# Performance work log

Hardware: AMD Instinct MI355X
Metric: run time of the kernel (lower is better)

Reference implementation:

```python
import jax, jax.numpy as jnp
import numpy as np

# ---- fixed sizes ----
N_IN = 100_000          # total inner nodes
NODES_PER_INNER = 50    # nodes per inner graph
N_OUT = N_IN // NODES_PER_INNER          # 2000 outer nodes (= num inner graphs)
NODES_PER_OUTER = 125   # outer nodes per outer graph
B = N_OUT // NODES_PER_OUTER             # 16 graphs in the batch
DEG = 8
E_IN = N_IN * DEG        # 800_000 inner edges
E_OUT = N_OUT * DEG      # 16_000 outer edges
IN_FEATS = 64
OUT_FEATS = 64
H = 128                  # h_feats = [128]*6
NUM_CLASSES = 10


def _rand_edges(key, n_graphs, nodes_per_graph, edges_per_graph):
    """Random edges that stay inside each graph of a batched graph."""
    k1, k2 = jax.random.split(key)
    src_l = jax.random.randint(k1, (n_graphs, edges_per_graph), 0, nodes_per_graph)
    dst_l = jax.random.randint(k2, (n_graphs, edges_per_graph), 0, nodes_per_graph)
    off = (jnp.arange(n_graphs) * nodes_per_graph)[:, None]
    return ((src_l + off).reshape(-1).astype(jnp.int32),
            (dst_l + off).reshape(-1).astype(jnp.int32))


def setup_inputs() -> dict:
    key = jax.random.key(0)
    ks = jax.random.split(key, 24)
    inner_src, inner_dst = _rand_edges(ks[0], N_OUT, NODES_PER_INNER, E_IN // N_OUT)
    outer_src, outer_dst = _rand_edges(ks[1], B, NODES_PER_OUTER, E_OUT // B)

    def w(k, fan_in, fan_out):
        return jax.random.normal(k, (fan_in, fan_out), jnp.float32) * (1.0 / np.sqrt(fan_in))

    inp = {
        "in_layer_feat": jax.random.normal(ks[2], (N_IN, IN_FEATS), jnp.float32),
        "out_layer_feat": jax.random.normal(ks[3], (N_OUT, OUT_FEATS), jnp.float32),
        "inner_ew": jax.random.uniform(ks[4], (E_IN,), jnp.float32) + 0.5,
        "outer_ew": jax.random.uniform(ks[5], (E_OUT,), jnp.float32) + 0.5,
        "W1": w(ks[6], IN_FEATS, H),        "b1": jnp.zeros((H,), jnp.float32),
        "W2": w(ks[7], H, H),               "b2": jnp.zeros((H,), jnp.float32),
        "W3": w(ks[8], OUT_FEATS + H, H),   "b3": jnp.zeros((H,), jnp.float32),
        "W4": w(ks[9], H, H),               "b4": jnp.zeros((H,), jnp.float32),
        "W5": w(ks[10], H, H),              "b5": jnp.zeros((H,), jnp.float32),
        "W6": w(ks[11], H, H),              "b6": jnp.zeros((H,), jnp.float32),
        "Wc": w(ks[12], H, NUM_CLASSES),    "bc": jnp.zeros((NUM_CLASSES,), jnp.float32),
        "inner_src": inner_src, "inner_dst": inner_dst,
        "outer_src": outer_src, "outer_dst": outer_dst,
        "inner_node_graph": (jnp.arange(N_IN) // NODES_PER_INNER).astype(jnp.int32),
        "outer_node_graph": (jnp.arange(N_OUT) // NODES_PER_OUTER).astype(jnp.int32),
    }
    return inp


def graph_conv(src, dst, ew, x, W, b, n_nodes):
    """DGL GraphConv, norm='both', weighted aggregation, zero-in-degree allowed."""
    ones = jnp.ones(src.shape[0], x.dtype)
    deg_out = jnp.clip(jax.ops.segment_sum(ones, src, num_segments=n_nodes), 1.0)
    deg_in = jnp.clip(jax.ops.segment_sum(ones, dst, num_segments=n_nodes), 1.0)
    xs = x * jax.lax.rsqrt(deg_out)[:, None]                      # src normalization
    msg = xs[src] * ew[:, None]                                   # u_mul_e
    agg = jax.ops.segment_sum(msg, dst, num_segments=n_nodes)     # copy_e -> sum
    agg = agg * jax.lax.rsqrt(deg_in)[:, None]                    # dst normalization
    return agg @ W + b


def mean_nodes(h, node_graph, n_graphs, nodes_per_graph):
    return jax.ops.segment_sum(h, node_graph, num_segments=n_graphs) / nodes_per_graph


def reference(in_layer_feat, out_layer_feat, inner_ew, outer_ew,
              W1, b1, W2, b2, W3, b3, W4, b4, W5, b5, W6, b6, Wc, bc,
              inner_src, inner_dst, outer_src, outer_dst,
              inner_node_graph, outer_node_graph):
    # inner-graph message passing
    h = jax.nn.relu(graph_conv(inner_src, inner_dst, inner_ew, in_layer_feat, W1, b1, N_IN))
    h = jax.nn.relu(graph_conv(inner_src, inner_dst, inner_ew, h, W2, b2, N_IN))
    reduced = mean_nodes(h, inner_node_graph, N_OUT, float(NODES_PER_INNER))  # [N_OUT, H]
    merged = jnp.concatenate([out_layer_feat, reduced], axis=-1)              # [N_OUT, OUT_FEATS+H]
    # outer-graph message passing
    h = jax.nn.relu(graph_conv(outer_src, outer_dst, outer_ew, merged, W3, b3, N_OUT))
    h = jax.nn.relu(graph_conv(outer_src, outer_dst, outer_ew, h, W4, b4, N_OUT))
    h = jax.nn.relu(graph_conv(outer_src, outer_dst, outer_ew, h, W5, b5, N_OUT))
    h = jax.nn.relu(graph_conv(outer_src, outer_dst, outer_ew, h, W6, b6, N_OUT))
    hg = mean_nodes(h, outer_node_graph, B, float(NODES_PER_OUTER))           # [B, H]
    return hg @ Wc + bc                                                       # [B, NUM_CLASSES]
```

## Files before the change

kernel.cpp:

```cpp
#include <hip/hip_runtime.h>

#define NPI 50
#define EPI 400
#define NPO 125
#define EPO 1000
#define N_IN 100000
#define N_OUT 2000
#define NB 16
#define NC 10

typedef _Float16 half_t;
typedef _Float16 f16x8 __attribute__((ext_vector_type(8)));
typedef _Float16 f16x4 __attribute__((ext_vector_type(4)));
typedef float f32x4 __attribute__((ext_vector_type(4)));

#define MFMA(a, b, c) __builtin_amdgcn_mfma_f32_16x16x32_f16(a, b, c, 0, 0, 0)

__device__ __forceinline__ void lds_barrier() {
    asm volatile("s_waitcnt lgkmcnt(0)" ::: "memory");
    __builtin_amdgcn_s_barrier();
}

__device__ __forceinline__ f16x8 lds_ld8(const half_t* base, int row, int k, int strideB) {
    return *(const f16x8*)((const char*)base + row * strideB + ((k * 2) ^ ((row & 7) << 4)));
}
__device__ __forceinline__ void lds_st1(half_t* base, int row, int col, int strideB, float v) {
    *(half_t*)((char*)base + row * strideB + ((col * 2) ^ ((row & 7) << 4))) = (half_t)v;
}
__device__ __forceinline__ void lds_st1h(half_t* base, int row, int col, int strideB, half_t v) {
    *(half_t*)((char*)base + row * strideB + ((col * 2) ^ ((row & 7) << 4))) = v;
}
__device__ __forceinline__ void lds_st4h(half_t* base, int row, int col0, int strideB, f16x4 v) {
    *(f16x4*)((char*)base + row * strideB + ((col0 * 2) ^ ((row & 7) << 4))) = v;
}
__device__ __forceinline__ f16x8 scr_ld8(const half_t* base, int row, int k) {
    return *(const f16x8*)((const char*)base + row * 64 + ((k * 2) ^ ((row & 3) << 4)));
}
__device__ __forceinline__ void scr_st1(half_t* base, int row, int col, float v) {
    *(half_t*)((char*)base + row * 64 + ((col * 2) ^ ((row & 3) << 4))) = (half_t)v;
}

__global__ __launch_bounds__(256) void k_pre(
    const float* __restrict__ W1, const float* __restrict__ W2,
    const float* __restrict__ W3, const float* __restrict__ W4,
    const float* __restrict__ W5, const float* __restrict__ W6,
    half_t* __restrict__ WT1, half_t* __restrict__ WT2,
    half_t* __restrict__ WT3, half_t* __restrict__ WT4,
    half_t* __restrict__ WT5, half_t* __restrict__ WT6,
    const float* __restrict__ ew, const int* __restrict__ esrc,
    const int* __restrict__ edst, half_t* __restrict__ Aout)
{
    __shared__ float Af[NPO * NPO];
    __shared__ int cO[NPO], cI[NPO];
    __shared__ float rso[NPO], rsi[NPO];
    const int t = threadIdx.x;

    if (blockIdx.x < 384) {
        int i = blockIdx.x * 256 + t;
        const float* src; half_t* dst; int K;
        if      (i < 8192)  { src = W1; dst = WT1; K = 64; }
        else if (i < 24576) { src = W2; dst = WT2; K = 128; i -= 8192; }
        else if (i < 49152) { src = W3; dst = WT3; K = 192; i -= 24576; }
        else if (i < 65536) { src = W4; dst = WT4; K = 128; i -= 49152; }
        else if (i < 81920) { src = W5; dst = WT5; K = 128; i -= 65536; }
        else                { src = W6; dst = WT6; K = 128; i -= 81920; }
        int c = i & 127, k = i >> 7;
        dst[c * K + k] = (half_t)src[k * 128 + c];
        return;
    }

    const int g = blockIdx.x - 384;
    const int nb = g * NPO, eb = g * EPO;
    for (int i = t; i < NPO * NPO; i += 256) Af[i] = 0.f;
    if (t < NPO) { cO[t] = 0; cI[t] = 0; }
    __syncthreads();
    for (int e = t; e < EPO; e += 256) {
        int s = esrc[eb + e] - nb, d = edst[eb + e] - nb;
        atomicAdd(&Af[d * NPO + s], ew[eb + e]);
        atomicAdd(&cO[s], 1); atomicAdd(&cI[d], 1);
    }
    __syncthreads();
    if (t < NPO) {
        rso[t] = rsqrtf((float)max(cO[t], 1));
        rsi[t] = rsqrtf((float)max(cI[t], 1));
    }
    __syncthreads();
    for (int i = t; i < 128 * 16; i += 256) {
        int d = i >> 4, s0 = (i & 15) * 8;
        f16x8 v;
        #pragma unroll
        for (int j = 0; j < 8; j++) {
            int s = s0 + j;
            float x = (d < NPO && s < NPO) ? Af[d * NPO + s] * rsi[d] * rso[s] : 0.f;
            v[j] = (half_t)x;
        }
        *(f16x8*)&Aout[(size_t)g * 16384 + d * 128 + s0] = v;
    }
}

__global__ __launch_bounds__(256, 5) void k_inner(
    const float* __restrict__ X, const float* __restrict__ outfeat,
    const float* __restrict__ ew, const int* __restrict__ esrc,
    const int* __restrict__ edst,
    const half_t* __restrict__ WT1, const float* __restrict__ b1,
    const half_t* __restrict__ WT2, const float* __restrict__ b2,
    half_t* __restrict__ merged)
{
    __shared__ alignas(16) char smem[21504];
    half_t* R2  = (half_t*)smem;
    float*  Af  = (float*)smem;
    half_t* scr = (half_t*)(smem + 16384);
    float*  pool= (float*)(smem + 20480);
    int*    cO  = (int*)(smem + 20992);
    int*    cI  = (int*)(smem + 21248);

    const int g = blockIdx.x, t = threadIdx.x;
    const int w = t >> 6, l = t & 63, lr = l & 15, lk = l >> 4;
    const int nb = g * NPI, eb = g * EPI;
    half_t* scrw = scr + w * 512;

    float ofv = (t < 64) ? outfeat[(size_t)g * 64 + t] : 0.f;
    int s0e, d0e; float w0e;
    { int e = eb + t; s0e = esrc[e] - nb; d0e = edst[e] - nb; w0e = ew[e]; }
    int s1e = 0, d1e = 0; float w1e = 0.f;
    const bool e1v = (t + 256 < EPI);
    if (e1v) { int e = eb + t + 256; s1e = esrc[e] - nb; d1e = edst[e] - nb; w1e = ew[e]; }
    f16x8 bx[8];
    #pragma unroll
    for (int fi = 0; fi < 4; fi++) {
        #pragma unroll
        for (int ks = 0; ks < 2; ks++) {
            f16x8 v;
            #pragma unroll
            for (int jj = 0; jj < 8; jj++) {
                int n = ks * 32 + lk * 8 + jj;
                int ridx = nb + n; if (ridx > N_IN - 1) ridx = N_IN - 1;
                v[jj] = (half_t)X[(size_t)ridx * 64 + fi * 16 + lr];
            }
            bx[fi * 2 + ks] = v;
        }
    }

    if (t < 64) { cO[t] = 0; cI[t] = 0; }
    if (t >= 64 && t < 192) pool[t - 64] = 0.f;
    {
        const f32x4 z4 = {0.f, 0.f, 0.f, 0.f};
        #pragma unroll
        for (int i = 0; i < 4; i++) *(f32x4*)&Af[(i * 256 + t) * 4] = z4;
    }
    lds_barrier();

    atomicAdd(&Af[d0e * 64 + (s0e ^ ((d0e & 7) << 2))], w0e);
    atomicAdd(&cO[s0e], 1); atomicAdd(&cI[d0e], 1);
    if (e1v) {
        atomicAdd(&Af[d1e * 64 + (s1e ^ ((d1e & 7) << 2))], w1e);
        atomicAdd(&cO[s1e], 1); atomicAdd(&cI[d1e], 1);
    }
    lds_barrier();

    f16x8 afr[2];
    {
        const int r = w * 16 + lr;
        const int sw = (r & 7) << 2;
        const float rsi_l = rsqrtf((float)max(cI[r], 1));
        #pragma unroll
        for (int ks = 0; ks < 2; ks++) {
            const int c0 = ks * 32 + lk * 8;
            f32x4 v0 = *(const f32x4*)&Af[r * 64 + (c0 ^ sw)];
            f32x4 v1 = *(const f32x4*)&Af[r * 64 + ((c0 + 4) ^ sw)];
            f16x8 fr;
            #pragma unroll
            for (int j = 0; j < 4; j++)
                fr[j] = (half_t)(v0[j] * rsi_l * rsqrtf((float)max(cO[c0 + j], 1)));
            #pragma unroll
            for (int j = 0; j < 4; j++)
                fr[4 + j] = (half_t)(v1[j] * rsi_l * rsqrtf((float)max(cO[c0 + 4 + j], 1)));
            afr[ks] = fr;
        }
    }
    lds_barrier();

    f32x4 hacc[8] = {};
    #pragma unroll
    for (int kf = 0; kf < 2; kf++) {
        f16x8 wb[8];
        #pragma unroll
        for (int nt = 0; nt < 8; nt++)
            wb[nt] = *(const f16x8*)&WT1[(nt * 16 + lr) * 64 + kf * 32 + lk * 8];
        #pragma unroll
        for (int j = 0; j < 2; j++) {
            const int ft = kf * 2 + j;
            f32x4 tacc = {};
            #pragma unroll
            for (int ks = 0; ks < 2; ks++)
                tacc = MFMA(afr[ks], bx[ft * 2 + ks], tacc);
            #pragma unroll
            for (int q = 0; q < 4; q++) scr_st1(scrw, lk * 4 + q, j * 16 + lr, tacc[q]);
        }
        f16x8 a1 = scr_ld8(scrw, lr, lk * 8);
        #pragma unroll
        for (int nt = 0; nt < 8; nt++) hacc[nt] = MFMA(a1, wb[nt], hacc[nt]);
    }
    #pragma unroll
    for (int nt = 0; nt < 8; nt++) {
        int c = nt * 16 + lr;
        float bb = b1[c];
        f16x4 hv;
        #pragma unroll
        for (int q = 0; q < 4; q++) hv[q] = (half_t)fmaxf(hacc[nt][q] + bb, 0.f);
        lds_st4h(R2, c, w * 16 + lk * 4, 128, hv);
    }
    lds_barrier();

    f32x4 h2[8] = {};
    #pragma unroll
    for (int kf = 0; kf < 4; kf++) {
        f16x8 wb[8];
        #pragma unroll
        for (int nt = 0; nt < 8; nt++)
            wb[nt] = *(const f16x8*)&WT2[(nt * 16 + lr) * 128 + kf * 32 + lk * 8];
        #pragma unroll
        for (int j = 0; j < 2; j++) {
            const int ft = kf * 2 + j;
            f32x4 tacc = {};
            #pragma unroll
            for (int ks = 0; ks < 2; ks++) {
                f16x8 b = lds_ld8(R2, ft * 16 + lr, ks * 32 + lk * 8, 128);
                tacc = MFMA(afr[ks], b, tacc);
            }
            #pragma unroll
            for (int q = 0; q < 4; q++) scr_st1(scrw, lk * 4 + q, j * 16 + lr, tacc[q]);
        }
        f16x8 a1 = scr_ld8(scrw, lr, lk * 8);
        #pragma unroll
        for (int nt = 0; nt < 8; nt++) h2[nt] = MFMA(a1, wb[nt], h2[nt]);
    }
    #pragma unroll
    for (int nt = 0; nt < 8; nt++) {
        int c = nt * 16 + lr;
        float bb = b2[c];
        float ps = 0.f;
        #pragma unroll
        for (int q = 0; q < 4; q++) {
            int m = w * 16 + lk * 4 + q;
            float v = fmaxf(h2[nt][q] + bb, 0.f);
            ps += (m < NPI) ? v : 0.f;
        }
        ps += __shfl_xor(ps, 16);
        ps += __shfl_xor(ps, 32);
        if (lk == 0) atomicAdd(&pool[c], ps);
    }
    lds_barrier();
    if (t < 64) merged[(size_t)g * 192 + t] = (half_t)ofv;
    else if (t < 192) merged[(size_t)g * 192 + t] = (half_t)(pool[t - 64] * (1.f / NPI));
}

template <int FIN, bool STAGE, bool LAST>
__device__ __forceinline__ void outer_layer(
    const f16x8* afr, const half_t* __restrict__ mg,
    const half_t* __restrict__ WT, const float* __restrict__ bias,
    half_t* bufP, half_t* bufQ, float* pool,
    int wr, int wc, int lr, int lk, int t)
{
    f32x4 hacc[4] = {};
    constexpr int NCH = FIN / 64;
    f16x8 hv[NCH];
    if constexpr (STAGE) {
        const int s = t >> 3, fo = (t & 7) * 8;
        #pragma unroll
        for (int ch = 0; ch < NCH; ch++) {
            f16x8 z = {};
            hv[ch] = (s < NPO) ? *(const f16x8*)&mg[(size_t)s * 192 + ch * 64 + fo] : z;
        }
    }
    #pragma unroll
    for (int ch = 0; ch < NCH; ch++) {
        f16x8 wtb[8];
        #pragma unroll
        for (int ks2 = 0; ks2 < 2; ks2++)
            #pragma unroll
            for (int nt = 0; nt < 4; nt++)
                wtb[ks2 * 4 + nt] = *(const f16x8*)&WT[
                    (size_t)(wc * 64 + nt * 16 + lr) * FIN + ch * 64 + ks2 * 32 + lk * 8];
        if constexpr (STAGE) {
            const int s = t >> 3, fo = (t & 7) * 8;
            #pragma unroll
            for (int j = 0; j < 8; j++) lds_st1h(bufP, fo + j, s, 256, hv[ch][j]);
            lds_barrier();
        }
        const int rb = STAGE ? 0 : ch * 64;
        f32x4 tacc[2] = {};
        #pragma unroll
        for (int ks = 0; ks < 4; ks++) {
            #pragma unroll
            for (int nt = 0; nt < 2; nt++) {
                f16x8 b = lds_ld8(bufP, rb + wc * 32 + nt * 16 + lr, ks * 32 + lk * 8, 256);
                tacc[nt] = MFMA(afr[ks], b, tacc[nt]);
            }
        }
        #pragma unroll
        for (int nt = 0; nt < 2; nt++)
            #pragma unroll
            for (int q = 0; q < 4; q++)
                lds_st1(bufQ, wr * 16 + lk * 4 + q, wc * 32 + nt * 16 + lr, 128,
                        tacc[nt][q]);
        lds_barrier();
        #pragma unroll
        for (int ks2 = 0; ks2 < 2; ks2++) {
            f16x8 a1 = lds_ld8(bufQ, wr * 16 + lr, ks2 * 32 + lk * 8, 128);
            #pragma unroll
            for (int nt = 0; nt < 4; nt++)
                hacc[nt] = MFMA(a1, wtb[ks2 * 4 + nt], hacc[nt]);
        }
        lds_barrier();
    }
    if constexpr (!LAST) {
        #pragma unroll
        for (int nt = 0; nt < 4; nt++) {
            int c = wc * 64 + nt * 16 + lr;
            float bb = bias[c];
            #pragma unroll
            for (int q = 0; q < 4; q++)
                lds_st1(bufP, c, wr * 16 + lk * 4 + q, 256, fmaxf(hacc[nt][q] + bb, 0.f));
        }
        lds_barrier();
    } else {
        #pragma unroll
        for (int nt = 0; nt < 4; nt++) {
            int c = wc * 64 + nt * 16 + lr;
            float bb = bias[c];
            float ps = 0.f;
            #pragma unroll
            for (int q = 0; q < 4; q++) {
                int d = wr * 16 + lk * 4 + q;
                float v = fmaxf(hacc[nt][q] + bb, 0.f);
                ps += (d < NPO) ? v : 0.f;
            }
            ps += __shfl_xor(ps, 16);
            ps += __shfl_xor(ps, 32);
            if (lk == 0) atomicAdd(&pool[c], ps);
        }
        lds_barrier();
    }
}

__global__ __launch_bounds__(1024) void k_outer(
    const half_t* __restrict__ Aout, const half_t* __restrict__ merged,
    const half_t* __restrict__ WT3, const float* __restrict__ b3,
    const half_t* __restrict__ WT4, const float* __restrict__ b4,
    const half_t* __restrict__ WT5, const float* __restrict__ b5,
    const half_t* __restrict__ WT6, const float* __restrict__ b6,
    const float* __restrict__ Wc, const float* __restrict__ bc,
    float* __restrict__ out)
{
    __shared__ alignas(16) char smem[49704];
    half_t* bufP = (half_t*)smem;
    half_t* bufQ = (half_t*)(smem + 32768);
    float*  pool = (float*)(smem + 49152);
    float*  cls  = (float*)(smem + 49664);

    const int g = blockIdx.x, t = threadIdx.x;
    const int w = t >> 6, l = t & 63, lr = l & 15, lk = l >> 4;
    const int wr = w & 7, wc = w >> 3;
    const half_t* mg = merged + (size_t)g * NPO * 192;

    f16x8 afr[4];
    #pragma unroll
    for (int ks = 0; ks < 4; ks++)
        afr[ks] = *(const f16x8*)&Aout[(size_t)g * 16384
                                       + (wr * 16 + lr) * 128 + ks * 32 + lk * 8];
    if (t < 128) pool[t] = 0.f;
    if (t >= 128 && t < 128 + NC) cls[t - 128] = 0.f;
    lds_barrier();

    outer_layer<192, true,  false>(afr, mg, WT3, b3, bufP, bufQ, pool, wr, wc, lr, lk, t);
    outer_layer<128, false, false>(afr, nullptr, WT4, b4, bufP, bufQ, pool, wr, wc, lr, lk, t);
    outer_layer<128, false, false>(afr, nullptr, WT5, b5, bufP, bufQ, pool, wr, wc, lr, lk, t);
    outer_layer<128, false, true >(afr, nullptr, WT6, b6, bufP, bufQ, pool, wr, wc, lr, lk, t);

    if (t < 128) {
        float val = pool[t] * (1.f / NPO);
        float p[NC];
        #pragma unroll
        for (int c = 0; c < NC; c++) p[c] = val * Wc[t * NC + c];
        #pragma unroll
        for (int off = 32; off >= 1; off >>= 1)
            #pragma unroll
            for (int c = 0; c < NC; c++) p[c] += __shfl_xor(p[c], off);
        if ((t & 63) == 0)
            #pragma unroll
            for (int c = 0; c < NC; c++) atomicAdd(&cls[c], p[c]);
    }
    lds_barrier();
    if (t < NC) out[g * NC + t] = cls[t] + bc[t];
}

extern "C" void kernel_launch(void* const* d_in, const int* in_sizes, int n_in,
                              void* d_out, int out_size, void* d_ws, size_t ws_size,
                              hipStream_t stream)
{
    const float* X       = (const float*)d_in[0];
    const float* outfeat = (const float*)d_in[1];
    const float* iew     = (const float*)d_in[2];
    const float* oew     = (const float*)d_in[3];
    const float* W1 = (const float*)d_in[4];  const float* b1 = (const float*)d_in[5];
    const float* W2 = (const float*)d_in[6];  const float* b2 = (const float*)d_in[7];
    const float* W3 = (const float*)d_in[8];  const float* b3 = (const float*)d_in[9];
    const float* W4 = (const float*)d_in[10]; const float* b4 = (const float*)d_in[11];
    const float* W5 = (const float*)d_in[12]; const float* b5 = (const float*)d_in[13];
    const float* W6 = (const float*)d_in[14]; const float* b6 = (const float*)d_in[15];
    const float* Wc = (const float*)d_in[16]; const float* bc = (const float*)d_in[17];
    const int* isrc = (const int*)d_in[18];   const int* idst = (const int*)d_in[19];
    const int* osrc = (const int*)d_in[20];   const int* odst = (const int*)d_in[21];

    char* base = (char*)d_ws;
    half_t* WT1 = (half_t*)(base + 0);
    half_t* WT2 = (half_t*)(base + 16384);
    half_t* WT3 = (half_t*)(base + 49152);
    half_t* WT4 = (half_t*)(base + 98304);
    half_t* WT5 = (half_t*)(base + 131072);
    half_t* WT6 = (half_t*)(base + 163840);
    half_t* AoutG  = (half_t*)(base + 196608);
    half_t* merged = (half_t*)(base + 720896);

    k_pre<<<400, 256, 0, stream>>>(W1, W2, W3, W4, W5, W6,
                                   WT1, WT2, WT3, WT4, WT5, WT6,
                                   oew, osrc, odst, AoutG);
    k_inner<<<N_OUT, 256, 0, stream>>>(X, outfeat, iew, isrc, idst,
                                       WT1, b1, WT2, b2, merged);
    k_outer<<<NB, 1024, 0, stream>>>(AoutG, merged, WT3, b3, WT4, b4,
                                     WT5, b5, WT6, b6, Wc, bc, (float*)d_out);
}
```

Before: 115.9 us.

## Restructure outer-graph layers to per-wave row ownership with private LDS scratch

The outer kernel moves from 1024 threads, split into 8 row waves by 2 column waves, to 512 threads where each wave owns 16 destination rows and all 128 output columns. Each wave writes its aggregated A·H tile to a private padded LDS scratch, so the barriers between the aggregation and weight-multiply stages inside each feature chunk go away. Only one barrier per layer remains around the shared activation buffer. In exchange LDS use roughly doubles, each wave streams the full weight matrix from global memory inside the MFMA loop, and per-block thread parallelism is halved.

```diff
diff --git a/kernel.cpp b/kernel.cpp
--- a/kernel.cpp
+++ b/kernel.cpp
@@ -38,6 +38,12 @@
 }
 __device__ __forceinline__ void scr_st1(half_t* base, int row, int col, float v) {
     *(half_t*)((char*)base + row * 64 + ((col * 2) ^ ((row & 3) << 4))) = (half_t)v;
+}
+__device__ __forceinline__ f16x8 scrS_ld8(const half_t* base, int row, int k, int strideB) {
+    return *(const f16x8*)((const char*)base + row * strideB + ((k * 2) ^ ((row & 3) << 4)));
+}
+__device__ __forceinline__ void scrS_st1(half_t* base, int row, int col, int strideB, float v) {
+    *(half_t*)((char*)base + row * strideB + ((col * 2) ^ ((row & 3) << 4))) = (half_t)v;
 }
 
 __global__ __launch_bounds__(256) void k_pre(
@@ -256,83 +262,67 @@
 }
 
 template <int FIN, bool STAGE, bool LAST>
-__device__ __forceinline__ void outer_layer(
+__device__ __forceinline__ void olayer(
     const f16x8* afr, const half_t* __restrict__ mg,
     const half_t* __restrict__ WT, const float* __restrict__ bias,
-    half_t* bufP, half_t* bufQ, float* pool,
-    int wr, int wc, int lr, int lk, int t)
+    half_t* bufP, half_t* scrw, float* pool,
+    int w, int lr, int lk, int t)
 {
-    f32x4 hacc[4] = {};
-    constexpr int NCH = FIN / 64;
-    f16x8 hv[NCH];
+    constexpr int SSTR = FIN * 2 + 16;
     if constexpr (STAGE) {
-        const int s = t >> 3, fo = (t & 7) * 8;
-        #pragma unroll
-        for (int ch = 0; ch < NCH; ch++) {
-            f16x8 z = {};
-            hv[ch] = (s < NPO) ? *(const f16x8*)&mg[(size_t)s * 192 + ch * 64 + fo] : z;
-        }
-    }
-    #pragma unroll
-    for (int ch = 0; ch < NCH; ch++) {
-        f16x8 wtb[8];
-        #pragma unroll
-        for (int ks2 = 0; ks2 < 2; ks2++)
-            #pragma unroll
-            for (int nt = 0; nt < 4; nt++)
-                wtb[ks2 * 4 + nt] = *(const f16x8*)&WT[
-                    (size_t)(wc * 64 + nt * 16 + lr) * FIN + ch * 64 + ks2 * 32 + lk * 8];
-        if constexpr (STAGE) {
-            const int s = t >> 3, fo = (t & 7) * 8;
-            #pragma unroll
-            for (int j = 0; j < 8; j++) lds_st1h(bufP, fo + j, s, 256, hv[ch][j]);
-            lds_barrier();
-        }
-        const int rb = STAGE ? 0 : ch * 64;
-        f32x4 tacc[2] = {};
+        const int s = t & 127, ch = t >> 7;
+        #pragma unroll
+        for (int j = 0; j < 6; j++) {
+            int f0 = ch * 48 + j * 8;
+            f16x8 hv = {};
+            if (s < NPO) hv = *(const f16x8*)&mg[(size_t)s * 192 + f0];
+            #pragma unroll
+            for (int i = 0; i < 8; i++) lds_st1h(bufP, f0 + i, s, 256, hv[i]);
+        }
+        lds_barrier();
+    }
+    #pragma unroll
+    for (int ft = 0; ft < FIN / 16; ft++) {
+        f32x4 tacc = {};
         #pragma unroll
         for (int ks = 0; ks < 4; ks++) {
-            #pragma unroll
-            for (int nt = 0; nt < 2; nt++) {
-                f16x8 b = lds_ld8(bufP, rb + wc * 32 + nt * 16 + lr, ks * 32 + lk * 8, 256);
-                tacc[nt] = MFMA(afr[ks], b, tacc[nt]);
-            }
-        }
-        #pragma unroll
-        for (int nt = 0; nt < 2; nt++)
+            f16x8 b = lds_ld8(bufP, ft * 16 + lr, ks * 32 + lk * 8, 256);
+            tacc = MFMA(afr[ks], b, tacc);
+        }
+        #pragma unroll
+        for (int q = 0; q < 4; q++)
+            scrS_st1(scrw, lk * 4 + q, ft * 16 + lr, SSTR, tacc[q]);
+    }
+    f32x4 hacc[8] = {};
+    #pragma unroll
+    for (int kf = 0; kf < FIN / 32; kf++) {
+        f16x8 a1 = scrS_ld8(scrw, lr, kf * 32 + lk * 8, SSTR);
+        #pragma unroll
+        for (int nt = 0; nt < 8; nt++) {
+            f16x8 wb = *(const f16x8*)&WT[(size_t)(nt * 16 + lr) * FIN + kf * 32 + lk * 8];
+            hacc[nt] = MFMA(a1, wb, hacc[nt]);
+        }
+    }
+    lds_barrier();
+    if constexpr (!LAST) {
+        #pragma unroll
+        for (int nt = 0; nt < 8; nt++) {
+            int c = nt * 16 + lr;
+            float bb = bias[c];
             #pragma unroll
             for (int q = 0; q < 4; q++)
-                lds_st1(bufQ, wr * 16 + lk * 4 + q, wc * 32 + nt * 16 + lr, 128,
-                        tacc[nt][q]);
-        lds_barrier();
-        #pragma unroll
-        for (int ks2 = 0; ks2 < 2; ks2++) {
-            f16x8 a1 = lds_ld8(bufQ, wr * 16 + lr, ks2 * 32 + lk * 8, 128);
-            #pragma unroll
-            for (int nt = 0; nt < 4; nt++)
-                hacc[nt] = MFMA(a1, wtb[ks2 * 4 + nt], hacc[nt]);
-        }
-        lds_barrier();
-    }
-    if constexpr (!LAST) {
-        #pragma unroll
-        for (int nt = 0; nt < 4; nt++) {
-            int c = wc * 64 + nt * 16 + lr;
-            float bb = bias[c];
-            #pragma unroll
-            for (int q = 0; q < 4; q++)
-                lds_st1(bufP, c, wr * 16 + lk * 4 + q, 256, fmaxf(hacc[nt][q] + bb, 0.f));
+                lds_st1(bufP, c, w * 16 + lk * 4 + q, 256, fmaxf(hacc[nt][q] + bb, 0.f));
         }
         lds_barrier();
     } else {
         #pragma unroll
-        for (int nt = 0; nt < 4; nt++) {
-            int c = wc * 64 + nt * 16 + lr;
+        for (int nt = 0; nt < 8; nt++) {
+            int c = nt * 16 + lr;
             float bb = bias[c];
             float ps = 0.f;
             #pragma unroll
             for (int q = 0; q < 4; q++) {
-                int d = wr * 16 + lk * 4 + q;
+                int d = w * 16 + lk * 4 + q;
                 float v = fmaxf(hacc[nt][q] + bb, 0.f);
                 ps += (d < NPO) ? v : 0.f;
             }
@@ -344,7 +334,7 @@
     }
 }
 
-__global__ __launch_bounds__(1024) void k_outer(
+__global__ __launch_bounds__(512) void k_outer(
     const half_t* __restrict__ Aout, const half_t* __restrict__ merged,
     const half_t* __restrict__ WT3, const float* __restrict__ b3,
     const half_t* __restrict__ WT4, const float* __restrict__ b4,
@@ -353,30 +343,29 @@
     const float* __restrict__ Wc, const float* __restrict__ bc,
     float* __restrict__ out)
 {
-    __shared__ alignas(16) char smem[49704];
+    __shared__ alignas(16) char smem[100928];
     half_t* bufP = (half_t*)smem;
-    half_t* bufQ = (half_t*)(smem + 32768);
-    float*  pool = (float*)(smem + 49152);
-    float*  cls  = (float*)(smem + 49664);
+    float*  pool = (float*)(smem + 100352);
+    float*  cls  = (float*)(smem + 100864);
 
     const int g = blockIdx.x, t = threadIdx.x;
     const int w = t >> 6, l = t & 63, lr = l & 15, lk = l >> 4;
-    const int wr = w & 7, wc = w >> 3;
+    half_t* scrw = (half_t*)(smem + 49152 + w * 6400);
     const half_t* mg = merged + (size_t)g * NPO * 192;
 
     f16x8 afr[4];
     #pragma unroll
     for (int ks = 0; ks < 4; ks++)
         afr[ks] = *(const f16x8*)&Aout[(size_t)g * 16384
-                                       + (wr * 16 + lr) * 128 + ks * 32 + lk * 8];
+                                       + (w * 16 + lr) * 128 + ks * 32 + lk * 8];
     if (t < 128) pool[t] = 0.f;
     if (t >= 128 && t < 128 + NC) cls[t - 128] = 0.f;
     lds_barrier();
 
-    outer_layer<192, true,  false>(afr, mg, WT3, b3, bufP, bufQ, pool, wr, wc, lr, lk, t);
-    outer_layer<128, false, false>(afr, nullptr, WT4, b4, bufP, bufQ, pool, wr, wc, lr, lk, t);
-    outer_layer<128, false, false>(afr, nullptr, WT5, b5, bufP, bufQ, pool, wr, wc, lr, lk, t);
-    outer_layer<128, false, true >(afr, nullptr, WT6, b6, bufP, bufQ, pool, wr, wc, lr, lk, t);
+    olayer<192, true,  false>(afr, mg, WT3, b3, bufP, scrw, pool, w, lr, lk, t);
+    olayer<128, false, false>(afr, nullptr, WT4, b4, bufP, scrw, pool, w, lr, lk, t);
+    olayer<128, false, false>(afr, nullptr, WT5, b5, bufP, scrw, pool, w, lr, lk, t);
+    olayer<128, false, true >(afr, nullptr, WT6, b6, bufP, scrw, pool, w, lr, lk, t);
 
     if (t < 128) {
         float val = pool[t] * (1.f / NPO);
@@ -428,6 +417,6 @@
                                    oew, osrc, odst, AoutG);
     k_inner<<<N_OUT, 256, 0, stream>>>(X, outfeat, iew, isrc, idst,
                                        WT1, b1, WT2, b2, merged);
-    k_outer<<<NB, 1024, 0, stream>>>(AoutG, merged, WT3, b3, WT4, b4,
-                                     WT5, b5, WT6, b6, Wc, bc, (float*)d_out);
-}
+    k_outer<<<NB, 512, 0, stream>>>(AoutG, merged, WT3, b3, WT4, b4,
+                                    WT5, b5, WT6, b6, Wc, bc, (float*)d_out);
+}
```

New measurement: 120.3 us. 3.8% more time.

## Pre-transpose inner node features to fp16 in prep kernel for vector loads

Applied to the files above, without the earlier changes.

Adds 1000 blocks to the prep kernel that stage X through LDS and write a per-graph transposed, zero-padded fp16 copy (64x64 per inner graph). The inner kernel then loads its MFMA B operands with 16-byte vector loads instead of 64 strided scalar fp32 loads per thread. The prep kernel's LDS use grows to about 64KB and rsi becomes a per-thread computation. In exchange there is an extra global write and read of the transposed features (about 16MB of traffic), and the prep kernel's occupancy drops.

```diff
diff --git a/kernel.cpp b/kernel.cpp
--- a/kernel.cpp
+++ b/kernel.cpp
@@ -48,11 +48,15 @@
     half_t* __restrict__ WT3, half_t* __restrict__ WT4,
     half_t* __restrict__ WT5, half_t* __restrict__ WT6,
     const float* __restrict__ ew, const int* __restrict__ esrc,
-    const int* __restrict__ edst, half_t* __restrict__ Aout)
+    const int* __restrict__ edst, half_t* __restrict__ Aout,
+    const float* __restrict__ X, half_t* __restrict__ XTG)
 {
-    __shared__ float Af[NPO * NPO];
-    __shared__ int cO[NPO], cI[NPO];
-    __shared__ float rso[NPO], rsi[NPO];
+    __shared__ alignas(16) char psm[64256];
+    float* Af  = (float*)psm;
+    float* Xs  = (float*)psm;
+    int*   cO  = (int*)(psm + 62500);
+    int*   cI  = (int*)(psm + 63000);
+    float* rso = (float*)(psm + 63500);
     const int t = threadIdx.x;
 
     if (blockIdx.x < 384) {
@@ -69,6 +73,27 @@
         return;
     }
 
+    if (blockIdx.x >= 400) {
+        const int g0 = (blockIdx.x - 400) * 2;
+        for (int i = t; i < 100 * 16; i += 256) {
+            int row = i >> 4, q = (i & 15) * 4;
+            *(float4*)&Xs[row * 64 + q] =
+                *(const float4*)&X[(size_t)(g0 * NPI + row) * 64 + q];
+        }
+        __syncthreads();
+        for (int i = t; i < 2 * 64 * 8; i += 256) {
+            int gg = i >> 9, f = (i >> 3) & 63, n0 = (i & 7) * 8;
+            f16x8 v;
+            #pragma unroll
+            for (int j = 0; j < 8; j++) {
+                int n = n0 + j;
+                v[j] = (n < NPI) ? (half_t)Xs[(gg * NPI + n) * 64 + f] : (half_t)0.f;
+            }
+            *(f16x8*)&XTG[(size_t)(g0 + gg) * 4096 + f * 64 + n0] = v;
+        }
+        return;
+    }
+
     const int g = blockIdx.x - 384;
     const int nb = g * NPO, eb = g * EPO;
     for (int i = t; i < NPO * NPO; i += 256) Af[i] = 0.f;
@@ -80,18 +105,16 @@
         atomicAdd(&cO[s], 1); atomicAdd(&cI[d], 1);
     }
     __syncthreads();
-    if (t < NPO) {
-        rso[t] = rsqrtf((float)max(cO[t], 1));
-        rsi[t] = rsqrtf((float)max(cI[t], 1));
-    }
+    if (t < NPO) rso[t] = rsqrtf((float)max(cO[t], 1));
     __syncthreads();
     for (int i = t; i < 128 * 16; i += 256) {
         int d = i >> 4, s0 = (i & 15) * 8;
+        float rsi_l = (d < NPO) ? rsqrtf((float)max(cI[d], 1)) : 0.f;
         f16x8 v;
         #pragma unroll
         for (int j = 0; j < 8; j++) {
             int s = s0 + j;
-            float x = (d < NPO && s < NPO) ? Af[d * NPO + s] * rsi[d] * rso[s] : 0.f;
+            float x = (d < NPO && s < NPO) ? Af[d * NPO + s] * rsi_l * rso[s] : 0.f;
             v[j] = (half_t)x;
         }
         *(f16x8*)&Aout[(size_t)g * 16384 + d * 128 + s0] = v;
@@ -99,7 +122,7 @@
 }
 
 __global__ __launch_bounds__(256, 5) void k_inner(
-    const float* __restrict__ X, const float* __restrict__ outfeat,
+    const half_t* __restrict__ XTG, const float* __restrict__ outfeat,
     const float* __restrict__ ew, const int* __restrict__ esrc,
     const int* __restrict__ edst,
     const half_t* __restrict__ WT1, const float* __restrict__ b1,
@@ -126,19 +149,14 @@
     const bool e1v = (t + 256 < EPI);
     if (e1v) { int e = eb + t + 256; s1e = esrc[e] - nb; d1e = edst[e] - nb; w1e = ew[e]; }
     f16x8 bx[8];
-    #pragma unroll
-    for (int fi = 0; fi < 4; fi++) {
-        #pragma unroll
-        for (int ks = 0; ks < 2; ks++) {
-            f16x8 v;
-            #pragma unroll
-            for (int jj = 0; jj < 8; jj++) {
-                int n = ks * 32 + lk * 8 + jj;
-                int ridx = nb + n; if (ridx > N_IN - 1) ridx = N_IN - 1;
-                v[jj] = (half_t)X[(size_t)ridx * 64 + fi * 16 + lr];
-            }
-            bx[fi * 2 + ks] = v;
-        }
+    {
+        const half_t* xtg = XTG + (size_t)g * 4096;
+        #pragma unroll
+        for (int fi = 0; fi < 4; fi++)
+            #pragma unroll
+            for (int ks = 0; ks < 2; ks++)
+                bx[fi * 2 + ks] =
+                    *(const f16x8*)&xtg[(fi * 16 + lr) * 64 + ks * 32 + lk * 8];
     }
 
     if (t < 64) { cO[t] = 0; cI[t] = 0; }
@@ -422,11 +440,12 @@
     half_t* WT6 = (half_t*)(base + 163840);
     half_t* AoutG  = (half_t*)(base + 196608);
     half_t* merged = (half_t*)(base + 720896);
-
-    k_pre<<<400, 256, 0, stream>>>(W1, W2, W3, W4, W5, W6,
-                                   WT1, WT2, WT3, WT4, WT5, WT6,
-                                   oew, osrc, odst, AoutG);
-    k_inner<<<N_OUT, 256, 0, stream>>>(X, outfeat, iew, isrc, idst,
+    half_t* XTG    = (half_t*)(base + 1490944);
+
+    k_pre<<<1400, 256, 0, stream>>>(W1, W2, W3, W4, W5, W6,
+                                    WT1, WT2, WT3, WT4, WT5, WT6,
+                                    oew, osrc, odst, AoutG, X, XTG);
+    k_inner<<<N_OUT, 256, 0, stream>>>(XTG, outfeat, iew, isrc, idst,
                                        WT1, b1, WT2, b2, merged);
     k_outer<<<NB, 1024, 0, stream>>>(AoutG, merged, WT3, b3, WT4, b4,
                                      WT5, b5, WT6, b6, Wc, bc, (float*)d_out);
```

New measurement: 123.2 us. 6.3% more time.
